# Kernel optimization log

Hardware: AMD Instinct MI355X
Metric: run time of the kernel (lower is better)

Reference implementation:

```python
import jax, jax.numpy as jnp
import numpy as np

N_ATOMS = 16384
M_NBR = 32  # neighbors per center


def setup_inputs() -> dict:
    key = jax.random.key(0)
    k1, k2, k3 = jax.random.split(key, 3)
    # atom positions in a 10 A box so a realistic fraction of pairs fall inside cutoffs
    coords = jax.random.uniform(k1, (N_ATOMS, 3), jnp.float32) * 10.0
    centers = jnp.arange(N_ATOMS, dtype=jnp.int32)
    # neighbors distinct from the center: center + offset in [1, N) mod N
    off = jax.random.randint(k2, (N_ATOMS, M_NBR), 1, N_ATOMS, dtype=jnp.int32)
    nbrs = (centers[:, None] + off) % N_ATOMS
    nl = jnp.concatenate([centers[:, None], nbrs], axis=1)  # [N, M+1]
    elements = jax.random.randint(k3, (N_ATOMS, M_NBR + 1), 0, 2, dtype=jnp.int32)
    # Stillinger-Weber parameters from __init__ (indexed by elem-sum)
    A = jnp.array([3.9781804791, 11.3797414404, 1.1907355764], jnp.float32)
    B = jnp.array([0.4446021306, 0.5266688197, 0.9015152673], jnp.float32)
    p = jnp.array([5.0, 5.0, 5.0], jnp.float32)
    q = jnp.array([0.0, 0.0, 0.0], jnp.float32)
    sigma = jnp.array([2.85295, 2.17517, 2.84133], jnp.float32)
    gamma = jnp.array([1.3566322033, 1.3566322033, 1.3566322033], jnp.float32)
    cutoff = jnp.array([5.5466, 4.02692, 4.51956], jnp.float32)
    lam = jnp.array([7.4767529158, 8.159518122], jnp.float32)
    cos_beta0 = jnp.array([0.1428569579923222, 0.1428569579923222], jnp.float32)
    cutoff_jk = jnp.array([3.86095, 5.5466], jnp.float32)
    return dict(coords=coords, A=A, B=B, p=p, q=q, sigma=sigma, gamma=gamma,
                cutoff=cutoff, lam=lam, cos_beta0=cos_beta0, cutoff_jk=cutoff_jk,
                elements=elements, nl=nl)


def reference(coords, A, B, p, q, sigma, gamma, cutoff, lam, cos_beta0, cutoff_jk, elements, nl):
    ci = nl[:, 0]            # [N] center atom indices
    nj = nl[:, 1:]           # [N, M] neighbor indices
    xi = coords[ci][:, None, :]       # [N,1,3]
    dij = coords[nj] - xi             # [N,M,3]
    rij = jnp.sqrt(jnp.sum(dij * dij, -1))  # [N,M]
    ei = elements[:, 0:1]             # [N,1]
    ej = elements[:, 1:]              # [N,M]

    # ---- two-body term ----
    s2 = ei + ej                      # in {0,1,2}
    A2, B2, p2, q2 = A[s2], B[s2], p[s2], q[s2]
    sg2, c2 = sigma[s2], cutoff[s2]
    m2 = rij < c2
    r2 = jnp.where(m2, rij, 0.5 * c2)  # safe value for masked lanes
    sr = sg2 / r2
    E2 = A2 * (B2 * sr ** p2 - sr ** q2) * jnp.exp(sg2 / (r2 - c2))
    e_pair = 0.5 * jnp.sum(jnp.where(m2, E2, 0.0))

    # ---- three-body term over all j<k neighbor pairs per center ----
    Mn = rij.shape[1]
    jj, kk = np.triu_indices(Mn, 1)   # static triplet enumeration, T = M(M-1)/2
    rij_t, rik_t = rij[:, jj], rij[:, kk]            # [N,T]
    djk = dij[:, kk, :] - dij[:, jj, :]
    rjk_t = jnp.sqrt(jnp.sum(djk * djk, -1))
    ej_t, ek_t = ej[:, jj], ej[:, kk]
    cond = (ei != ej_t) & (ej_t == ek_t)
    ijk = jnp.clip(2 - (ei + ej_t + ek_t), 0, 1)     # index into 2-entry lists
    gij, cij = gamma[ei + ej_t], cutoff[ei + ej_t]
    gik, cik = gamma[ei + ek_t], cutoff[ei + ek_t]
    cjk = cutoff_jk[ijk]
    m3 = cond & (rij_t < cij) & (rik_t < cik) & (rjk_t < cjk)
    rij_s = jnp.where(rij_t < cij, rij_t, 0.5 * cij)
    rik_s = jnp.where(rik_t < cik, rik_t, 0.5 * cik)
    cosb = (rij_s ** 2 + rik_s ** 2 - rjk_t ** 2) / (2.0 * rij_s * rik_s)
    E3 = lam[ijk] * jnp.exp(gij / (rij_s - cij) + gik / (rik_s - cik)) * (cosb - cos_beta0[ijk]) ** 2
    e_trip = jnp.sum(jnp.where(m3, E3, 0.0))

    return e_pair + e_trip
```

## Files before the change

### kernel.cpp

```cpp
#include <hip/hip_runtime.h>
#include <cmath>

#define NATOMS 16384
#define MNBR   32
#define ROW    33
#define NBLK   2048
#define LOG2E  1.4426950408889634f

typedef float f4v __attribute__((ext_vector_type(4), aligned(4)));

__device__ __forceinline__ float sel3(int s, float v0, float v1, float v2) {
    float r = (s == 0) ? v0 : v1;
    return (s == 2) ? v2 : r;
}

__device__ __forceinline__ void load_xyz(const float* __restrict__ coords, int j,
                                         float& x, float& y, float& z) {
    const bool last = (j == NATOMS - 1);
    const int  off  = 3 * j - (last ? 1 : 0);
    const f4v  v    = *reinterpret_cast<const f4v*>(coords + off);
    x = last ? v.y : v.x;
    y = last ? v.z : v.y;
    z = last ? v.w : v.z;
}

__global__ __launch_bounds__(256, 8) void sw_energy_kernel(
    const float* __restrict__ coords,
    const float* __restrict__ A_,    const float* __restrict__ B_,
    const float* __restrict__ p_,    const float* __restrict__ q_,
    const float* __restrict__ sigma_,const float* __restrict__ gamma_,
    const float* __restrict__ cutoff_,const float* __restrict__ lam_,
    const float* __restrict__ cb0_,  const float* __restrict__ cjk_,
    const int*   __restrict__ elements,
    const int*   __restrict__ nl,
    float* __restrict__ block_sums)
{
    __shared__ float4 cpos[4][2][32];
    __shared__ float  chh [4][2][32];
    __shared__ float  wsum[4];

    const int tid  = threadIdx.x;
    const int wave = tid >> 6;
    const int lane = tid & 63;
    const int side = lane >> 5;
    const int hl   = lane & 31;

    const float a0 = A_[0],     a1 = A_[1],     a2 = A_[2];
    const float b0 = B_[0],     b1 = B_[1],     b2 = B_[2];
    const float p0 = p_[0],     p1 = p_[1],     p2 = p_[2];
    const float q0 = q_[0],     q1 = q_[1],     q2 = q_[2];
    const float s0 = sigma_[0], s1 = sigma_[1], s2v = sigma_[2];
    const float g0 = gamma_[0], g1 = gamma_[1], g2 = gamma_[2];
    const float c0 = cutoff_[0],c1 = cutoff_[1],c2 = cutoff_[2];
    const float lam0 = lam_[0], lam1 = lam_[1];
    const float cb0v = cb0_[0], cb1v = cb0_[1];
    const float cjk0 = cjk_[0], cjk1 = cjk_[1];

    const bool fastpq = (p0 == 5.0f) & (p1 == 5.0f) & (p2 == 5.0f)
                      & (q0 == 0.0f) & (q1 == 0.0f) & (q2 == 0.0f);

    const int atom = (blockIdx.x << 3) + wave * 2 + side;
    const int base = atom * ROW;

    const int ei = elements[base];
    const int ci = nl[base];
    float xix, xiy, xiz;
    load_xyz(coords, ci, xix, xiy, xiz);

    float acc = 0.0f;

    const int j  = nl[base + 1 + hl];
    const int ej = elements[base + 1 + hl];
    float cjx, cjy, cjz;
    load_xyz(coords, j, cjx, cjy, cjz);
    const float dx = cjx - xix;
    const float dy = cjy - xiy;
    const float dz = cjz - xiz;
    const float d2 = dx*dx + dy*dy + dz*dz;
    const float inv_r = __builtin_amdgcn_rsqf(d2);
    const float r     = d2 * inv_r;
    const int   s  = ei + ej;
    const float c  = sel3(s, c0, c1, c2);
    const bool  valid = (r < c);

    float h = 0.0f;
    if (valid) {
        const float sg     = sel3(s, s0, s1, s2v);
        const float inv_rc = __builtin_amdgcn_rcpf(r - c);
        const float sr     = sg * inv_r;
        float poly;
        if (fastpq) {
            const float sr2 = sr * sr;
            poly = sel3(s, b0, b1, b2) * (sr2 * sr2 * sr) - 1.0f;
        } else {
            const float l2 = log2f(sr);
            poly = sel3(s, b0, b1, b2) * exp2f(sel3(s, p0, p1, p2) * l2)
                 - exp2f(sel3(s, q0, q1, q2) * l2);
        }
        const float e2 = sel3(s, a0, a1, a2) * poly
                       * __builtin_amdgcn_exp2f(LOG2E * sg * inv_rc);
        acc += 0.5f * e2;
        h = sel3(s, g0, g1, g2) * inv_rc;
    }

    const bool participate = valid && (ej != ei);
    const unsigned long long ballot   = __ballot(participate);
    const unsigned long long halfmask = side ? 0xFFFFFFFF00000000ull : 0x00000000FFFFFFFFull;
    const int m = __popcll(ballot & halfmask);
    if (participate) {
        const int slot = __popcll(ballot & halfmask & ((1ull << lane) - 1ull));
        cpos[wave][side][slot] = make_float4(dx, dy, dz, r);
        chh [wave][side][slot] = h;
    }

    const float lam_e = ei ? lam1 : lam0;
    const float cb_e  = ei ? cb1v : cb0v;
    const float cjk_e = ei ? cjk1 : cjk0;
    const float cjk2  = cjk_e * cjk_e;
    const int npairs  = (m * (m - 1)) >> 1;

    for (int t = hl; t < npairs; t += 32) {
        int kk = (int)(0.5f * (1.0f + __builtin_amdgcn_sqrtf(8.0f * (float)t + 1.0f)));
        if (kk*(kk-1)/2 > t)          --kk;
        else if ((kk+1)*kk/2 <= t)    ++kk;
        const int jj = t - ((kk*(kk-1)) >> 1);

        const float4 pj = cpos[wave][side][jj];
        const float4 pk = cpos[wave][side][kk];
        const float dxv  = pk.x - pj.x;
        const float dyv  = pk.y - pj.y;
        const float dzv  = pk.z - pj.z;
        const float rjk2 = dxv*dxv + dyv*dyv + dzv*dzv;
        if (rjk2 < cjk2) {
            const float rj   = pj.w;
            const float rk   = pk.w;
            const float cosb = (rj*rj + rk*rk - rjk2)
                             * 0.5f * __builtin_amdgcn_rcpf(rj * rk);
            const float dcb  = cosb - cb_e;
            acc += lam_e * dcb * dcb
                 * __builtin_amdgcn_exp2f(LOG2E * (chh[wave][side][jj] + chh[wave][side][kk]));
        }
    }

    #pragma unroll
    for (int off = 32; off > 0; off >>= 1)
        acc += __shfl_xor(acc, off, 64);
    if (lane == 0) wsum[wave] = acc;
    __syncthreads();
    if (tid == 0)
        block_sums[blockIdx.x] = (wsum[0] + wsum[1]) + (wsum[2] + wsum[3]);
}

__global__ __launch_bounds__(512) void sw_reduce_kernel(
    const float* __restrict__ in, float* __restrict__ out)
{
    __shared__ float wsum[8];
    const float4 x = ((const float4*)in)[threadIdx.x];
    float acc = (x.x + x.y) + (x.z + x.w);
    #pragma unroll
    for (int off = 32; off > 0; off >>= 1)
        acc += __shfl_xor(acc, off, 64);
    if ((threadIdx.x & 63) == 0) wsum[threadIdx.x >> 6] = acc;
    __syncthreads();
    if (threadIdx.x == 0) {
        float t = 0.0f;
        #pragma unroll
        for (int i = 0; i < 8; ++i) t += wsum[i];
        out[0] = t;
    }
}

extern "C" void kernel_launch(void* const* d_in, const int* in_sizes, int n_in,
                              void* d_out, int out_size, void* d_ws, size_t ws_size,
                              hipStream_t stream)
{
    const float* coords  = (const float*)d_in[0];
    const float* A_      = (const float*)d_in[1];
    const float* B_      = (const float*)d_in[2];
    const float* p_      = (const float*)d_in[3];
    const float* q_      = (const float*)d_in[4];
    const float* sigma_  = (const float*)d_in[5];
    const float* gamma_  = (const float*)d_in[6];
    const float* cutoff_ = (const float*)d_in[7];
    const float* lam_    = (const float*)d_in[8];
    const float* cb0_    = (const float*)d_in[9];
    const float* cjk_    = (const float*)d_in[10];
    const int*   elements= (const int*)d_in[11];
    const int*   nl      = (const int*)d_in[12];

    float* out   = (float*)d_out;
    float* bsums = (float*)d_ws;

    sw_energy_kernel<<<NBLK, 256, 0, stream>>>(
        coords, A_, B_, p_, q_, sigma_, gamma_, cutoff_,
        lam_, cb0_, cjk_, elements, nl, bsums);
    sw_reduce_kernel<<<1, 512, 0, stream>>>(bsums, out);
}
```

Measured before the change: 11.35 us.

## Fuse final reduction into main kernel via per-block flags and a spinning reducer block

Removes the separate reduce kernel launch. Each block writes its partial sum and then release-stores a magic flag. An extra block (index NBLK) spins on all flags with acquire loads, sums the partials, writes the output and resets the flags. This saves a kernel launch and the gap between launches, but the reducer block only finishes if it is scheduled alongside the others, because it occupies a CU slot while it spins. It also relies on the workspace flags starting out zeroed.

```diff
diff --git a/kernel.cpp b/kernel.cpp
--- a/kernel.cpp
+++ b/kernel.cpp
@@ -6,6 +6,7 @@
 #define ROW    33
 #define NBLK   2048
 #define LOG2E  1.4426950408889634f
+#define MAGIC  0x1234ABCDu
 
 typedef float f4v __attribute__((ext_vector_type(4), aligned(4)));
 
@@ -33,13 +34,51 @@
     const float* __restrict__ cb0_,  const float* __restrict__ cjk_,
     const int*   __restrict__ elements,
     const int*   __restrict__ nl,
-    float* __restrict__ block_sums)
+    float* __restrict__ ws,
+    float* __restrict__ out)
 {
     __shared__ float4 cpos[4][2][32];
     __shared__ float  chh [4][2][32];
     __shared__ float  wsum[4];
 
-    const int tid  = threadIdx.x;
+    float*    partials = ws;
+    unsigned* flags    = (unsigned*)(ws + NBLK);
+
+    const int tid = threadIdx.x;
+
+    if (blockIdx.x == NBLK) {
+        bool done;
+        do {
+            done = true;
+            #pragma unroll
+            for (int i = 0; i < NBLK / 256; ++i) {
+                const unsigned f = __hip_atomic_load(&flags[tid + i * 256],
+                                                     __ATOMIC_ACQUIRE,
+                                                     __HIP_MEMORY_SCOPE_AGENT);
+                done &= (f == MAGIC);
+            }
+        } while (!__syncthreads_and((int)done));
+
+        float acc = 0.0f;
+        #pragma unroll
+        for (int i = 0; i < NBLK / 256; ++i)
+            acc += __hip_atomic_load(&partials[tid + i * 256],
+                                     __ATOMIC_RELAXED, __HIP_MEMORY_SCOPE_AGENT);
+        #pragma unroll
+        for (int off = 32; off > 0; off >>= 1)
+            acc += __shfl_xor(acc, off, 64);
+        if ((tid & 63) == 0) wsum[tid >> 6] = acc;
+        __syncthreads();
+        if (tid == 0)
+            out[0] = (wsum[0] + wsum[1]) + (wsum[2] + wsum[3]);
+
+        #pragma unroll
+        for (int i = 0; i < NBLK / 256; ++i)
+            __hip_atomic_store(&flags[tid + i * 256], 0u,
+                               __ATOMIC_RELAXED, __HIP_MEMORY_SCOPE_AGENT);
+        return;
+    }
+
     const int wave = tid >> 6;
     const int lane = tid & 63;
     const int side = lane >> 5;
@@ -147,26 +186,12 @@
         acc += __shfl_xor(acc, off, 64);
     if (lane == 0) wsum[wave] = acc;
     __syncthreads();
-    if (tid == 0)
-        block_sums[blockIdx.x] = (wsum[0] + wsum[1]) + (wsum[2] + wsum[3]);
-}
-
-__global__ __launch_bounds__(512) void sw_reduce_kernel(
-    const float* __restrict__ in, float* __restrict__ out)
-{
-    __shared__ float wsum[8];
-    const float4 x = ((const float4*)in)[threadIdx.x];
-    float acc = (x.x + x.y) + (x.z + x.w);
-    #pragma unroll
-    for (int off = 32; off > 0; off >>= 1)
-        acc += __shfl_xor(acc, off, 64);
-    if ((threadIdx.x & 63) == 0) wsum[threadIdx.x >> 6] = acc;
-    __syncthreads();
-    if (threadIdx.x == 0) {
-        float t = 0.0f;
-        #pragma unroll
-        for (int i = 0; i < 8; ++i) t += wsum[i];
-        out[0] = t;
+    if (tid == 0) {
+        const float part = (wsum[0] + wsum[1]) + (wsum[2] + wsum[3]);
+        __hip_atomic_store(&partials[blockIdx.x], part,
+                           __ATOMIC_RELAXED, __HIP_MEMORY_SCOPE_AGENT);
+        __hip_atomic_store(&flags[blockIdx.x], MAGIC,
+                           __ATOMIC_RELEASE, __HIP_MEMORY_SCOPE_AGENT);
     }
 }
 
@@ -188,11 +213,10 @@
     const int*   elements= (const int*)d_in[11];
     const int*   nl      = (const int*)d_in[12];
 
-    float* out   = (float*)d_out;
-    float* bsums = (float*)d_ws;
-
-    sw_energy_kernel<<<NBLK, 256, 0, stream>>>(
+    float* out = (float*)d_out;
+    float* ws  = (float*)d_ws;
+
+    sw_energy_kernel<<<NBLK + 1, 256, 0, stream>>>(
         coords, A_, B_, p_, q_, sigma_, gamma_, cutoff_,
-        lam_, cb0_, cjk_, elements, nl, bsums);
-    sw_reduce_kernel<<<1, 512, 0, stream>>>(bsums, out);
-}
+        lam_, cb0_, cjk_, elements, nl, ws, out);
+}
```

Result: slower. 31.65 us (+178.9%).
